# Kernel optimization log

Measured on AMD Instinct MI355X. Metric: run time of the kernel, lower is better.

The kernel has to match this reference:

```python
import jax, jax.numpy as jnp
import numpy as np

# ---- model config (mirrors argparse args) ----
SW = 512          # signal_window_size
TSI = 1           # mf_time_slice_interval
MP = 2            # mf_maxpool_size
SUBW = 128        # subwindow_size
NBINS = (SW // TSI) // SUBW   # 4
NF = 48           # dwt_num_filters
NEG = 0.02        # LeakyReLU negative slope
SP = 8 // MP      # spatial size after maxpool = 4
J = 4             # dwt levels (pywt.dwt_max_level(128, 'db4'))
DWT_OUT_LEN = 154 # 14 (lo) + 14 + 22 + 37 + 67

# pywt 'db4' analysis filters
DEC_LO = np.array([-0.010597401784997278, 0.032883011666982945,
                   0.030841381835986965, -0.18703481171888114,
                   -0.02798376941698385, 0.6308807679295904,
                   0.7148465705525415, 0.23037781330885523], np.float32)
DEC_HI = np.array([-0.23037781330885523, 0.7148465705525415,
                   -0.6308807679295904, -0.02798376941698385,
                   0.18703481171888114, 0.030841381835986965,
                   -0.032883011666982945, -0.010597401784997278], np.float32)
# pytorch_wavelets reverses the pywt filters then applies cross-correlation
H0R = jnp.asarray(DEC_LO[::-1].copy())
H1R = jnp.asarray(DEC_HI[::-1].copy())


def _afb1d(x):
    """One DWT analysis level with reflect padding. x: (B, N) -> (lo, hi) each (B, out)."""
    L = H0R.shape[0]
    N = x.shape[-1]
    out = (N + L - 1) // 2                  # pywt.dwt_coeff_len, non-periodic mode
    p = 2 * (out - 1) - N + L
    xp = jnp.pad(x, ((0, 0), (p // 2, (p + 1) // 2)), mode='reflect')
    filt = jnp.stack([H0R, H1R])[:, None, :]        # (2, 1, L)
    y = jax.lax.conv_general_dilated(xp[:, None, :], filt,
                                     window_strides=(2,), padding='VALID')  # (B, 2, out)
    return y[:, 0, :], y[:, 1, :]


def _dwt_concat(x):
    """J-level DWT along last axis; concat [lo_J, hi_1, ..., hi_J]. x: (B, SUBW)."""
    his = []
    lo = x
    for _ in range(J):
        lo, hi = _afb1d(lo)
        his.append(hi)
    return jnp.concatenate([lo] + his, axis=-1)     # (B, DWT_OUT_LEN)


def setup_inputs() -> dict:
    key = jax.random.key(0)
    k1, k2, k3 = jax.random.split(key, 3)
    x = jax.random.normal(k1, (2048, 1, SW, 8, 8), dtype=jnp.float32)
    # per-subwindow Conv3d weights: kernel = (DWT_OUT_LEN, SP, SP) -> 1x1x1 output
    conv_w = jax.random.normal(k2, (NBINS, NF, DWT_OUT_LEN, SP, SP), dtype=jnp.float32) * 0.02
    conv_b = jax.random.normal(k3, (NBINS, NF), dtype=jnp.float32) * 0.02
    return {"x": x, "conv_w": conv_w, "conv_b": conv_b}


def reference(x, conv_w, conv_b):
    # x: (N, 1, SW, 8, 8)
    n = x.shape[0]
    x = x[:, :, ::TSI]                                   # time slicing (no-op for TSI=1)
    t = SW // TSI
    # MaxPool3d kernel (1, MP, MP)
    x = x.reshape(n, 1, t, SP, MP, SP, MP).max(axis=(4, 6))   # (N, 1, T, SP, SP)
    # split time into subwindows
    x = x.reshape(n, NBINS, SUBW, SP, SP)
    # DWT along time for every (batch, bin, h, w) signal, fully batched
    xb = x.transpose(0, 1, 3, 4, 2).reshape(-1, SUBW)         # (N*NBINS*SP*SP, SUBW)
    coeffs = _dwt_concat(xb).reshape(n, NBINS, SP, SP, DWT_OUT_LEN)
    # Conv3d with full-size kernel per subwindow == weighted reduction + bias
    feats = jnp.einsum('nbhwt,bfthw->nbf', coeffs, conv_w) + conv_b[None]  # (N, NBINS, NF)
    # dropout3d is identity in eval mode; LeakyReLU then flatten
    out = jax.nn.leaky_relu(feats, NEG).reshape(n, -1)        # (N, NBINS*NF)
    return out
```

## Files before the change

kernel.cpp:

```cpp
#include <hip/hip_runtime.h>


#define NBINS 4
#define NFEAT 48
#define DWT_LEN 154

__device__ __constant__ float c_h0r[8] = {
    0.23037781330885523f,  0.7148465705525415f,   0.6308807679295904f,
   -0.02798376941698385f, -0.18703481171888114f,  0.030841381835986965f,
    0.032883011666982945f, -0.010597401784997278f };
__device__ __constant__ float c_h1r[8] = {
   -0.010597401784997278f, -0.032883011666982945f, 0.030841381835986965f,
    0.18703481171888114f,  -0.02798376941698385f, -0.6308807679295904f,
    0.7148465705525415f,   -0.23037781330885523f };

__global__ void build_dwt_matrix(float* __restrict__ D) {
  __shared__ float work[128 * 64];
  __shared__ float tmp[67 * 64];
  int ls = threadIdx.x;
  int s  = blockIdx.x * 64 + ls;
  for (int i = 0; i < 128; ++i) work[i * 64 + ls] = (i == s) ? 1.f : 0.f;
  int N = 128;
  const int HI_OFF[4] = {14, 81, 118, 140};
  for (int lev = 0; lev < 4; ++lev) {
    int out = (N + 7) >> 1;
    int p  = 2 * (out - 1) - N + 8;
    int pl = p >> 1;
    for (int k = 0; k < out; ++k) {
      float lo = 0.f, hi = 0.f;
      #pragma unroll
      for (int l = 0; l < 8; ++l) {
        int idx = 2 * k + l - pl;
        idx = idx < 0 ? -idx : idx;
        idx = idx >= N ? 2 * N - 2 - idx : idx;
        float v = work[idx * 64 + ls];
        lo += c_h0r[l] * v;
        hi += c_h1r[l] * v;
      }
      tmp[k * 64 + ls] = lo;
      D[(HI_OFF[lev] + k) * 128 + s] = hi;
    }
    for (int k = 0; k < out; ++k) work[k * 64 + ls] = tmp[k * 64 + ls];
    N = out;
  }
  for (int k = 0; k < 14; ++k) D[k * 128 + s] = work[k * 64 + ls];
}

__global__ void build_weff(const float* __restrict__ conv_w,
                           const float* __restrict__ D,
                           float* __restrict__ Weff) {
  int bf = blockIdx.x;
  __shared__ float cw[DWT_LEN * 16];
  for (int i = threadIdx.x; i < DWT_LEN * 16; i += blockDim.x)
    cw[i] = conv_w[(size_t)bf * (DWT_LEN * 16) + i];
  __syncthreads();
  int s  = threadIdx.x & 127;
  int h0 = threadIdx.x >> 7;
  float acc[8] = {0.f, 0.f, 0.f, 0.f, 0.f, 0.f, 0.f, 0.f};
  #pragma unroll 4
  for (int t = 0; t < DWT_LEN; ++t) {
    float d = D[t * 128 + s];
    #pragma unroll
    for (int j = 0; j < 8; ++j) acc[j] += cw[t * 16 + h0 + 2 * j] * d;
  }
  #pragma unroll
  for (int j = 0; j < 8; ++j) {
    int hw = h0 + 2 * j;
    Weff[(size_t)bf * 2048 + s * 16 + hw] = acc[j];
  }
}

__global__ __launch_bounds__(256, 4)
void dwt_feat_main(const float* __restrict__ x,
                   const float* __restrict__ Weff,
                   const float* __restrict__ conv_b,
                   float* __restrict__ out, int n_total) {
  __shared__ float part[4][NFEAT][4];
  int lane = threadIdx.x & 63;
  int kq   = threadIdx.x >> 6;
  int b    = blockIdx.x & 3;
  int n0   = (blockIdx.x >> 2) * 4;
  if (n0 >= n_total) return;

  float4 pa[4][2];
  #pragma unroll
  for (int nn = 0; nn < 4; ++nn) {
    const float4* xs =
        (const float4*)(x + (size_t)(n0 + nn) * 32768 + (size_t)b * 8192);
    #pragma unroll
    for (int pp = 0; pp < 2; ++pp) {
      int fi = (kq * 2 + pp) * 256 + lane * 4;
      float4 a0 = xs[fi + 0], a1 = xs[fi + 1];
      float4 b0 = xs[fi + 2], b1 = xs[fi + 3];
      float4 pv;
      pv.x = fmaxf(fmaxf(a0.x, a0.y), fmaxf(b0.x, b0.y));
      pv.y = fmaxf(fmaxf(a0.z, a0.w), fmaxf(b0.z, b0.w));
      pv.z = fmaxf(fmaxf(a1.x, a1.y), fmaxf(b1.x, b1.y));
      pv.w = fmaxf(fmaxf(a1.z, a1.w), fmaxf(b1.z, b1.w));
      pa[nn][pp] = pv;
    }
  }

  const float4* W4 = (const float4*)(Weff + (size_t)b * NFEAT * 2048);
  for (int f = 0; f < NFEAT; ++f) {
    float acc0 = 0.f, acc1 = 0.f, acc2 = 0.f, acc3 = 0.f;
    #pragma unroll
    for (int pp = 0; pp < 2; ++pp) {
      float4 w = W4[f * 512 + (kq * 2 + pp) * 64 + lane];
      float4 p0 = pa[0][pp], p1 = pa[1][pp], p2 = pa[2][pp], p3 = pa[3][pp];
      acc0 += p0.x * w.x + p0.y * w.y + p0.z * w.z + p0.w * w.w;
      acc1 += p1.x * w.x + p1.y * w.y + p1.z * w.z + p1.w * w.w;
      acc2 += p2.x * w.x + p2.y * w.y + p2.z * w.z + p2.w * w.w;
      acc3 += p3.x * w.x + p3.y * w.y + p3.z * w.z + p3.w * w.w;
    }
    #pragma unroll
    for (int m = 32; m >= 1; m >>= 1) {
      acc0 += __shfl_xor(acc0, m, 64);
      acc1 += __shfl_xor(acc1, m, 64);
      acc2 += __shfl_xor(acc2, m, 64);
      acc3 += __shfl_xor(acc3, m, 64);
    }
    if (lane < 4) {
      float v = lane == 0 ? acc0 : lane == 1 ? acc1 : lane == 2 ? acc2 : acc3;
      part[kq][f][lane] = v;
    }
  }
  __syncthreads();

  int t = threadIdx.x;
  if (t < NFEAT * 4) {
    int f  = t % NFEAT;
    int nn = t / NFEAT;
    float v = part[0][f][nn] + part[1][f][nn] + part[2][f][nn] + part[3][f][nn];
    v += conv_b[b * NFEAT + f];
    v = v > 0.f ? v : 0.02f * v;
    out[(size_t)(n0 + nn) * (NBINS * NFEAT) + b * NFEAT + f] = v;
  }
}

extern "C" void kernel_launch(void* const* d_in, const int* in_sizes, int n_in,
                              void* d_out, int out_size, void* d_ws, size_t ws_size,
                              hipStream_t stream) {
  const float* x      = (const float*)d_in[0];
  const float* conv_w = (const float*)d_in[1];
  const float* conv_b = (const float*)d_in[2];
  float* out = (float*)d_out;

  float* D    = (float*)d_ws;
  float* Weff = (float*)d_ws + 32768;

  int n = in_sizes[0] / 32768;

  build_dwt_matrix<<<2, 64, 0, stream>>>(D);
  build_weff<<<NBINS * NFEAT, 256, 0, stream>>>(conv_w, D, Weff);
  dwt_feat_main<<<(n / 4) * NBINS, 256, 0, stream>>>(x, Weff, conv_b, out, n);
}
```

Baseline: 495.1 us.

## Restructure feature GEMM with double-buffered LDS staging via global_load_lds

Rewrites the main kernel as a small tiled GEMM. Each block handles 8 samples per bin. The K dimension is split into 64-wide chunks, and both the max-pooled activations and the Weff tiles are staged into double-buffered LDS. Weff tiles are copied asynchronously with global_load_lds into an XOR-swizzled layout, and the next chunk's x is prefetched while the current one is computed. Each thread accumulates 3 features for one sample, which removes the cross-lane shuffle reductions and doubles reuse of each Weff load, in exchange for one barrier per chunk, more LDS, and a smaller block.

```diff
diff --git a/kernel.cpp b/kernel.cpp
--- a/kernel.cpp
+++ b/kernel.cpp
@@ -1,9 +1,19 @@
 #include <hip/hip_runtime.h>
+#include <stdint.h>
 
 
 #define NBINS 4
 #define NFEAT 48
 #define DWT_LEN 154
+
+#define TN 8
+#define KC 64
+#define NCHUNK 32
+#define KROW 68
+#define WBYTES (NFEAT * KC * 4)
+
+#define GLOBAL_AS __attribute__((address_space(1)))
+#define LDS_AS __attribute__((address_space(3)))
 
 __device__ __constant__ float c_h0r[8] = {
     0.23037781330885523f,  0.7148465705525415f,   0.6308807679295904f,
@@ -70,72 +80,103 @@
   }
 }
 
-__global__ __launch_bounds__(256, 4)
+__global__ __launch_bounds__(128, 2)
 void dwt_feat_main(const float* __restrict__ x,
                    const float* __restrict__ Weff,
                    const float* __restrict__ conv_b,
                    float* __restrict__ out, int n_total) {
-  __shared__ float part[4][NFEAT][4];
-  int lane = threadIdx.x & 63;
-  int kq   = threadIdx.x >> 6;
-  int b    = blockIdx.x & 3;
-  int n0   = (blockIdx.x >> 2) * 4;
+  __shared__ __align__(16) float P_lds[2][TN][KROW];
+  __shared__ __align__(16) uint8_t W_lds[2][WBYTES];
+
+  const int tid  = threadIdx.x;
+  const int wave = tid >> 6;
+  const int b    = blockIdx.x & 3;
+  const int n0   = (blockIdx.x >> 2) * TN;
   if (n0 >= n_total) return;
 
-  float4 pa[4][2];
-  #pragma unroll
-  for (int nn = 0; nn < 4; ++nn) {
-    const float4* xs =
-        (const float4*)(x + (size_t)(n0 + nn) * 32768 + (size_t)b * 8192);
+  const int cn  = tid & 7;
+  const int cfg = tid >> 3;
+  const int f0  = cfg * 3;
+
+  const int sn    = tid >> 4;
+  const int idx16 = tid & 15;
+  const int t_sub = idx16 >> 2;
+  const int hq    = idx16 & 3;
+  const int pk    = t_sub * 16 + hq * 4;
+
+  const float* xb =
+      x + (size_t)(n0 + sn) * 32768 + (size_t)b * 8192 + idx16 * 16;
+  const uint8_t* wb = (const uint8_t*)(Weff + (size_t)b * NFEAT * 2048);
+
+  float4 xr[4];
+
+  auto loadX = [&](int c) {
+    const float4* s = (const float4*)(xb + c * 256);
     #pragma unroll
-    for (int pp = 0; pp < 2; ++pp) {
-      int fi = (kq * 2 + pp) * 256 + lane * 4;
-      float4 a0 = xs[fi + 0], a1 = xs[fi + 1];
-      float4 b0 = xs[fi + 2], b1 = xs[fi + 3];
-      float4 pv;
-      pv.x = fmaxf(fmaxf(a0.x, a0.y), fmaxf(b0.x, b0.y));
-      pv.y = fmaxf(fmaxf(a0.z, a0.w), fmaxf(b0.z, b0.w));
-      pv.z = fmaxf(fmaxf(a1.x, a1.y), fmaxf(b1.x, b1.y));
-      pv.w = fmaxf(fmaxf(a1.z, a1.w), fmaxf(b1.z, b1.w));
-      pa[nn][pp] = pv;
+    for (int i = 0; i < 4; ++i) xr[i] = s[i];
+  };
+  auto stageP = [&](int buf) {
+    float4 p;
+    p.x = fmaxf(fmaxf(xr[0].x, xr[0].y), fmaxf(xr[2].x, xr[2].y));
+    p.y = fmaxf(fmaxf(xr[0].z, xr[0].w), fmaxf(xr[2].z, xr[2].w));
+    p.z = fmaxf(fmaxf(xr[1].x, xr[1].y), fmaxf(xr[3].x, xr[3].y));
+    p.w = fmaxf(fmaxf(xr[1].z, xr[1].w), fmaxf(xr[3].z, xr[3].w));
+    *(float4*)&P_lds[buf][sn][pk] = p;
+  };
+  auto stageW = [&](int c, int buf) {
+    #pragma unroll
+    for (int r = 0; r < 6; ++r) {
+      uint32_t o = r * 2048 + tid * 16;
+      uint32_t f = o >> 8;
+      uint32_t inner = (o & 255) ^ ((f & 7) << 4);
+      const uint8_t* src = wb + f * 8192 + c * 256 + inner;
+      uint8_t* dst = &W_lds[buf][r * 2048 + wave * 1024];
+      __builtin_amdgcn_global_load_lds(
+          (const GLOBAL_AS uint32_t*)src, (LDS_AS uint32_t*)dst, 16, 0, 0);
     }
+  };
+
+  loadX(0);
+  stageW(0, 0);
+  stageP(0);
+  loadX(1);
+  __syncthreads();
+
+  const uint32_t wb0 = (uint32_t)(f0 + 0) << 8, xo0 = (uint32_t)((f0 + 0) & 7) << 4;
+  const uint32_t wb1 = (uint32_t)(f0 + 1) << 8, xo1 = (uint32_t)((f0 + 1) & 7) << 4;
+  const uint32_t wb2 = (uint32_t)(f0 + 2) << 8, xo2 = (uint32_t)((f0 + 2) & 7) << 4;
+
+  float acc0 = 0.f, acc1 = 0.f, acc2 = 0.f;
+
+  #pragma unroll 2
+  for (int c = 0; c < NCHUNK; ++c) {
+    const int cur = c & 1;
+    if (c + 1 < NCHUNK) {
+      stageW(c + 1, cur ^ 1);
+      stageP(cur ^ 1);
+      if (c + 2 < NCHUNK) loadX(c + 2);
+    }
+    const uint8_t* Wb = W_lds[cur];
+    const float*   Pb = P_lds[cur][cn];
+    #pragma unroll
+    for (int kk = 0; kk < 16; ++kk) {
+      float4 p = *(const float4*)(Pb + kk * 4);
+      uint32_t kx = (uint32_t)kk << 4;
+      float4 w0 = *(const float4*)(Wb + (wb0 | (kx ^ xo0)));
+      float4 w1 = *(const float4*)(Wb + (wb1 | (kx ^ xo1)));
+      float4 w2 = *(const float4*)(Wb + (wb2 | (kx ^ xo2)));
+      acc0 += p.x * w0.x + p.y * w0.y + p.z * w0.z + p.w * w0.w;
+      acc1 += p.x * w1.x + p.y * w1.y + p.z * w1.z + p.w * w1.w;
+      acc2 += p.x * w2.x + p.y * w2.y + p.z * w2.z + p.w * w2.w;
+    }
+    __syncthreads();
   }
 
-  const float4* W4 = (const float4*)(Weff + (size_t)b * NFEAT * 2048);
-  for (int f = 0; f < NFEAT; ++f) {
-    float acc0 = 0.f, acc1 = 0.f, acc2 = 0.f, acc3 = 0.f;
-    #pragma unroll
-    for (int pp = 0; pp < 2; ++pp) {
-      float4 w = W4[f * 512 + (kq * 2 + pp) * 64 + lane];
-      float4 p0 = pa[0][pp], p1 = pa[1][pp], p2 = pa[2][pp], p3 = pa[3][pp];
-      acc0 += p0.x * w.x + p0.y * w.y + p0.z * w.z + p0.w * w.w;
-      acc1 += p1.x * w.x + p1.y * w.y + p1.z * w.z + p1.w * w.w;
-      acc2 += p2.x * w.x + p2.y * w.y + p2.z * w.z + p2.w * w.w;
-      acc3 += p3.x * w.x + p3.y * w.y + p3.z * w.z + p3.w * w.w;
-    }
-    #pragma unroll
-    for (int m = 32; m >= 1; m >>= 1) {
-      acc0 += __shfl_xor(acc0, m, 64);
-      acc1 += __shfl_xor(acc1, m, 64);
-      acc2 += __shfl_xor(acc2, m, 64);
-      acc3 += __shfl_xor(acc3, m, 64);
-    }
-    if (lane < 4) {
-      float v = lane == 0 ? acc0 : lane == 1 ? acc1 : lane == 2 ? acc2 : acc3;
-      part[kq][f][lane] = v;
-    }
-  }
-  __syncthreads();
-
-  int t = threadIdx.x;
-  if (t < NFEAT * 4) {
-    int f  = t % NFEAT;
-    int nn = t / NFEAT;
-    float v = part[0][f][nn] + part[1][f][nn] + part[2][f][nn] + part[3][f][nn];
-    v += conv_b[b * NFEAT + f];
-    v = v > 0.f ? v : 0.02f * v;
-    out[(size_t)(n0 + nn) * (NBINS * NFEAT) + b * NFEAT + f] = v;
-  }
+  const float* bias = conv_b + b * NFEAT + f0;
+  float* o = out + (size_t)(n0 + cn) * (NBINS * NFEAT) + b * NFEAT + f0;
+  float v0 = acc0 + bias[0]; o[0] = v0 > 0.f ? v0 : 0.02f * v0;
+  float v1 = acc1 + bias[1]; o[1] = v1 > 0.f ? v1 : 0.02f * v1;
+  float v2 = acc2 + bias[2]; o[2] = v2 > 0.f ? v2 : 0.02f * v2;
 }
 
 extern "C" void kernel_launch(void* const* d_in, const int* in_sizes, int n_in,
@@ -153,5 +194,5 @@
 
   build_dwt_matrix<<<2, 64, 0, stream>>>(D);
   build_weff<<<NBINS * NFEAT, 256, 0, stream>>>(conv_w, D, Weff);
-  dwt_feat_main<<<(n / 4) * NBINS, 256, 0, stream>>>(x, Weff, conv_b, out, n);
+  dwt_feat_main<<<(n / TN) * NBINS, 128, 0, stream>>>(x, Weff, conv_b, out, n);
 }
```

Result: slower. 790.1 us (+59.6%).

## Restructure main kernel into LDS-staged chunked GEMM with register-blocked features

Applied to the files above, without the earlier changes.

Each block now handles 8 samples instead of 4. The pooled input is staged through a double-buffered LDS tile in 16 chunks of 128 elements, with the next chunk prefetched while the current one is consumed. Each thread computes 3 features for one sample over half of the K dimension, which replaces the per-feature 64-wide shuffle reductions with one LDS merge at the end. This cuts shuffle and reduction overhead and reuses each Weff load across more samples, at the cost of a barrier per chunk and a higher occupancy hint.

```diff
diff --git a/kernel.cpp b/kernel.cpp
--- a/kernel.cpp
+++ b/kernel.cpp
@@ -1,9 +1,15 @@
 #include <hip/hip_runtime.h>
+#include <stdint.h>
 
 
 #define NBINS 4
 #define NFEAT 48
 #define DWT_LEN 154
+
+#define TN 8
+#define CK 128
+#define NCHUNK 16
+#define PROW 132
 
 __device__ __constant__ float c_h0r[8] = {
     0.23037781330885523f,  0.7148465705525415f,   0.6308807679295904f,
@@ -70,71 +76,89 @@
   }
 }
 
-__global__ __launch_bounds__(256, 4)
+__global__ __launch_bounds__(256, 6)
 void dwt_feat_main(const float* __restrict__ x,
                    const float* __restrict__ Weff,
                    const float* __restrict__ conv_b,
                    float* __restrict__ out, int n_total) {
-  __shared__ float part[4][NFEAT][4];
-  int lane = threadIdx.x & 63;
-  int kq   = threadIdx.x >> 6;
-  int b    = blockIdx.x & 3;
-  int n0   = (blockIdx.x >> 2) * 4;
+  __shared__ __align__(16) float P_lds[2][TN][PROW];
+  __shared__ float Mrg[TN][16][3];
+
+  const int tid = threadIdx.x;
+  const int b   = blockIdx.x & 3;
+  const int n0  = (blockIdx.x >> 2) * TN;
   if (n0 >= n_total) return;
 
-  float4 pa[4][2];
-  #pragma unroll
-  for (int nn = 0; nn < 4; ++nn) {
-    const float4* xs =
-        (const float4*)(x + (size_t)(n0 + nn) * 32768 + (size_t)b * 8192);
-    #pragma unroll
-    for (int pp = 0; pp < 2; ++pp) {
-      int fi = (kq * 2 + pp) * 256 + lane * 4;
-      float4 a0 = xs[fi + 0], a1 = xs[fi + 1];
-      float4 b0 = xs[fi + 2], b1 = xs[fi + 3];
-      float4 pv;
-      pv.x = fmaxf(fmaxf(a0.x, a0.y), fmaxf(b0.x, b0.y));
-      pv.y = fmaxf(fmaxf(a0.z, a0.w), fmaxf(b0.z, b0.w));
-      pv.z = fmaxf(fmaxf(a1.x, a1.y), fmaxf(b1.x, b1.y));
-      pv.w = fmaxf(fmaxf(a1.z, a1.w), fmaxf(b1.z, b1.w));
-      pa[nn][pp] = pv;
+  const int sn      = tid >> 5;
+  const int q       = tid & 31;
+  const int s_local = q >> 2;
+  const int hp      = q & 3;
+  const float* xb = x + (size_t)(n0 + sn) * 32768 + (size_t)b * 8192
+                    + s_local * 64 + hp * 16;
+  const int pko = s_local * 16 + hp * 4;
+
+  const int n_c = tid & 7;
+  const int fg  = (tid >> 3) & 15;
+  const int kt  = tid >> 7;
+  const float* wbase =
+      Weff + ((size_t)b * NFEAT + fg * 3) * 2048 + kt * 64;
+
+  float4 xr0, xr1, xr2, xr3;
+  auto loadX = [&](int c) {
+    const float* p = xb + c * 512;
+    xr0 = *(const float4*)(p + 0);
+    xr1 = *(const float4*)(p + 4);
+    xr2 = *(const float4*)(p + 8);
+    xr3 = *(const float4*)(p + 12);
+  };
+  auto poolStore = [&](int buf) {
+    float4 pv;
+    pv.x = fmaxf(fmaxf(xr0.x, xr0.y), fmaxf(xr2.x, xr2.y));
+    pv.y = fmaxf(fmaxf(xr0.z, xr0.w), fmaxf(xr2.z, xr2.w));
+    pv.z = fmaxf(fmaxf(xr1.x, xr1.y), fmaxf(xr3.x, xr3.y));
+    pv.w = fmaxf(fmaxf(xr1.z, xr1.w), fmaxf(xr3.z, xr3.w));
+    *(float4*)&P_lds[buf][sn][pko] = pv;
+  };
+
+  float acc0 = 0.f, acc1 = 0.f, acc2 = 0.f;
+
+  loadX(0);
+  poolStore(0);
+  for (int c = 0; c < NCHUNK; ++c) {
+    __syncthreads();
+    if (c + 1 < NCHUNK) loadX(c + 1);
+    const float* Pb = &P_lds[c & 1][n_c][kt * 64];
+    const float* w0 = wbase + (size_t)c * CK;
+    const float* w1 = w0 + 2048;
+    const float* w2 = w0 + 4096;
+    #pragma unroll 4
+    for (int kk = 0; kk < 16; ++kk) {
+      float4 p  = *(const float4*)(Pb + kk * 4);
+      float4 wa = *(const float4*)(w0 + kk * 4);
+      float4 wbv = *(const float4*)(w1 + kk * 4);
+      float4 wc = *(const float4*)(w2 + kk * 4);
+      acc0 += p.x * wa.x + p.y * wa.y + p.z * wa.z + p.w * wa.w;
+      acc1 += p.x * wbv.x + p.y * wbv.y + p.z * wbv.z + p.w * wbv.w;
+      acc2 += p.x * wc.x + p.y * wc.y + p.z * wc.z + p.w * wc.w;
     }
+    if (c + 1 < NCHUNK) poolStore((c + 1) & 1);
   }
 
-  const float4* W4 = (const float4*)(Weff + (size_t)b * NFEAT * 2048);
-  for (int f = 0; f < NFEAT; ++f) {
-    float acc0 = 0.f, acc1 = 0.f, acc2 = 0.f, acc3 = 0.f;
-    #pragma unroll
-    for (int pp = 0; pp < 2; ++pp) {
-      float4 w = W4[f * 512 + (kq * 2 + pp) * 64 + lane];
-      float4 p0 = pa[0][pp], p1 = pa[1][pp], p2 = pa[2][pp], p3 = pa[3][pp];
-      acc0 += p0.x * w.x + p0.y * w.y + p0.z * w.z + p0.w * w.w;
-      acc1 += p1.x * w.x + p1.y * w.y + p1.z * w.z + p1.w * w.w;
-      acc2 += p2.x * w.x + p2.y * w.y + p2.z * w.z + p2.w * w.w;
-      acc3 += p3.x * w.x + p3.y * w.y + p3.z * w.z + p3.w * w.w;
-    }
-    #pragma unroll
-    for (int m = 32; m >= 1; m >>= 1) {
-      acc0 += __shfl_xor(acc0, m, 64);
-      acc1 += __shfl_xor(acc1, m, 64);
-      acc2 += __shfl_xor(acc2, m, 64);
-      acc3 += __shfl_xor(acc3, m, 64);
-    }
-    if (lane < 4) {
-      float v = lane == 0 ? acc0 : lane == 1 ? acc1 : lane == 2 ? acc2 : acc3;
-      part[kq][f][lane] = v;
-    }
+  if (kt == 1) {
+    Mrg[n_c][fg][0] = acc0;
+    Mrg[n_c][fg][1] = acc1;
+    Mrg[n_c][fg][2] = acc2;
   }
   __syncthreads();
-
-  int t = threadIdx.x;
-  if (t < NFEAT * 4) {
-    int f  = t % NFEAT;
-    int nn = t / NFEAT;
-    float v = part[0][f][nn] + part[1][f][nn] + part[2][f][nn] + part[3][f][nn];
-    v += conv_b[b * NFEAT + f];
-    v = v > 0.f ? v : 0.02f * v;
-    out[(size_t)(n0 + nn) * (NBINS * NFEAT) + b * NFEAT + f] = v;
+  if (kt == 0) {
+    const float* bias = conv_b + b * NFEAT + fg * 3;
+    float* o = out + (size_t)(n0 + n_c) * (NBINS * NFEAT) + b * NFEAT + fg * 3;
+    float v0 = acc0 + Mrg[n_c][fg][0] + bias[0];
+    float v1 = acc1 + Mrg[n_c][fg][1] + bias[1];
+    float v2 = acc2 + Mrg[n_c][fg][2] + bias[2];
+    o[0] = v0 > 0.f ? v0 : 0.02f * v0;
+    o[1] = v1 > 0.f ? v1 : 0.02f * v1;
+    o[2] = v2 > 0.f ? v2 : 0.02f * v2;
   }
 }
 
@@ -153,5 +177,5 @@
 
   build_dwt_matrix<<<2, 64, 0, stream>>>(D);
   build_weff<<<NBINS * NFEAT, 256, 0, stream>>>(conv_w, D, Weff);
-  dwt_feat_main<<<(n / 4) * NBINS, 256, 0, stream>>>(x, Weff, conv_b, out, n);
+  dwt_feat_main<<<(n / TN) * NBINS, 256, 0, stream>>>(x, Weff, conv_b, out, n);
 }
```

Result: faster. 471.9 us (-4.7%).
